# Optimization experiments

Measured on AMD Instinct MI355X. Metric: run time of the kernel, lower is better.

The kernel has to match this reference:

```python
import jax, jax.numpy as jnp
import numpy as np

EPS = 1e-5


def spectral_conv3d(x, w):
    # x: [B, C, X, Y, Z] real; w: [4, Cin, Cout, m1, m2, m3, 2] (4 frequency corners, real/imag)
    m1, m2, m3 = w.shape[3], w.shape[4], w.shape[5]
    wc = w[..., 0] + 1j * w[..., 1]
    X, Y, Z = x.shape[-3], x.shape[-2], x.shape[-1]
    xf = jnp.fft.rfftn(x, axes=(-3, -2, -1), norm="ortho")  # [B,C,X,Y,Z//2+1] complex
    mul = lambda a, b: jnp.einsum('bixyz,ioxyz->boxyz', a, b)
    out = jnp.zeros(xf.shape, dtype=xf.dtype)
    out = out.at[:, :, :m1, :m2, :m3].set(mul(xf[:, :, :m1, :m2, :m3], wc[0]))
    out = out.at[:, :, -m1:, :m2, :m3].set(mul(xf[:, :, -m1:, :m2, :m3], wc[1]))
    out = out.at[:, :, :m1, -m2:, :m3].set(mul(xf[:, :, :m1, -m2:, :m3], wc[2]))
    out = out.at[:, :, -m1:, -m2:, :m3].set(mul(xf[:, :, -m1:, -m2:, :m3], wc[3]))
    return jnp.fft.irfftn(out, s=(X, Y, Z), axes=(-3, -2, -1), norm="ortho")


def batchnorm3d(x, g, b):
    # training-mode BatchNorm3d: stats over (B, X, Y, Z) per channel, biased variance
    mean = jnp.mean(x, axis=(0, 2, 3, 4), keepdims=True)
    var = jnp.var(x, axis=(0, 2, 3, 4), keepdims=True)
    xhat = (x - mean) * jax.lax.rsqrt(var + EPS)
    return xhat * g[None, :, None, None, None] + b[None, :, None, None, None]


def setup_inputs() -> dict:
    key = jax.random.key(0)
    ks = jax.random.split(key, 12)
    B, X, Y, Z = 4, 64, 64, 64
    W, M = 32, 8
    scale = 1.0 / (W * W)
    return {
        "x": jax.random.normal(ks[0], (B, X, Y, Z, 3), dtype=jnp.float32),
        "fc0_w": jax.random.normal(ks[1], (W, 3), dtype=jnp.float32) * 0.3,
        "fc0_b": jax.random.normal(ks[2], (W,), dtype=jnp.float32) * 0.1,
        "sw": scale * jax.random.uniform(ks[3], (4, 4, W, W, M, M, M, 2), dtype=jnp.float32),
        "cw": jax.random.normal(ks[4], (4, W, W), dtype=jnp.float32) * (1.0 / np.sqrt(W)),
        "cb": jax.random.normal(ks[5], (4, W), dtype=jnp.float32) * 0.05,
        "gamma": jnp.ones((4, W), dtype=jnp.float32),
        "beta": jnp.zeros((4, W), dtype=jnp.float32),
        "fc1_w": jax.random.normal(ks[6], (128, W), dtype=jnp.float32) * (1.0 / np.sqrt(W)),
        "fc1_b": jax.random.normal(ks[7], (128,), dtype=jnp.float32) * 0.05,
        "fc2_w": jax.random.normal(ks[8], (1, 128), dtype=jnp.float32) * (1.0 / np.sqrt(128.0)),
        "fc2_b": jax.random.normal(ks[9], (1,), dtype=jnp.float32) * 0.05,
    }


def reference(x, fc0_w, fc0_b, sw, cw, cb, gamma, beta, fc1_w, fc1_b, fc2_w, fc2_b):
    # lift: [B,X,Y,Z,3] -> [B,X,Y,Z,W] -> [B,W,X,Y,Z]
    h = jnp.einsum('bxyzi,wi->bxyzw', x, fc0_w) + fc0_b
    h = jnp.transpose(h, (0, 4, 1, 2, 3))
    for i in range(4):
        x1 = spectral_conv3d(h, sw[i])
        x2 = jnp.einsum('bcxyz,oc->boxyz', h, cw[i]) + cb[i][None, :, None, None, None]
        h = batchnorm3d(x1 + x2, gamma[i], beta[i])
        if i < 3:
            h = jax.nn.relu(h)
    h = jnp.transpose(h, (0, 2, 3, 4, 1))  # [B,X,Y,Z,W]
    h = jax.nn.relu(jnp.einsum('bxyzw,fw->bxyzf', h, fc1_w) + fc1_b)
    out = jnp.einsum('bxyzf,of->bxyzo', h, fc2_w) + fc2_b
    return out
```

## Files before the change

kernel.cpp:

```cpp
#include <hip/hip_runtime.h>

#define TW_STEP 0.09817477042468103f

typedef __bf16 bf16x8 __attribute__((ext_vector_type(8)));
typedef __bf16 bf16x4 __attribute__((ext_vector_type(4)));
typedef __bf16 bf16x2 __attribute__((ext_vector_type(2)));
typedef float  f32x4  __attribute__((ext_vector_type(4)));

static constexpr size_t SZ_P   = (size_t)4*32*64*64*64*2;
static constexpr size_t SZ_A   = (size_t)4*32*8*64*64*8;
static constexpr size_t SZ_B2  = (size_t)4*32*8*16*64*8;
static constexpr size_t SZ_XF  = (size_t)4*32*8*16*16*8;
static constexpr size_t OFF_P  = 0;
static constexpr size_t OFF_A  = OFF_P + SZ_P;
static constexpr size_t OFF_B2 = OFF_A + SZ_A;
static constexpr size_t OFF_XF = OFF_B2 + SZ_B2;
static constexpr size_t OFF_YF = OFF_XF + SZ_XF;
static constexpr size_t OFF_TW  = OFF_YF + SZ_XF;
static constexpr size_t OFF_BNP = OFF_TW + 512;
static constexpr size_t OFF_W1B = OFF_BNP + 1024;
static constexpr size_t OFF_B1P = OFF_W1B + 8192;
static constexpr size_t OFF_WFZ = OFF_B1P + 512;
static constexpr size_t OFF_WZ  = OFF_WFZ + 4096;


__global__ void k_twinit(float2* tw, __bf16* wfz, __bf16* wz) {
    int t = threadIdx.x;
    if (t < 64) { float s, c; sincosf(TW_STEP * t, &s, &c); tw[t] = make_float2(c, s); }
    for (int e = t; e < 1024; e += 256) {
        int half = e >> 9, rem = e & 511, kg = rem >> 7, tt = (rem >> 3) & 15, j = e & 7;
        int z = half * 32 + kg * 8 + j, k = tt >> 1;
        float ang = TW_STEP * (float)((k * z) & 63);
        float val = (tt & 1) ? -sinf(ang) : cosf(ang);
        __bf16 hi = (__bf16)val;
        wfz[e] = hi;
        wfz[1024 + e] = (__bf16)(val - (float)hi);
    }
    for (int e = t; e < 2048; e += 256) {
        int z = e >> 5, tt = e & 31, k = tt >> 1;
        float ang = TW_STEP * (float)((k * z) & 63);
        float val;
        if (tt == 0) val = 1.f;
        else if (tt == 1) val = 0.f;
        else val = (tt & 1) ? (-2.f * sinf(ang)) : (2.f * cosf(ang));
        __bf16 hi = (__bf16)val;
        wz[e] = hi;
        wz[2048 + e] = (__bf16)(val - (float)hi);
    }
}

__global__ __launch_bounds__(256) void k_lift(const float* __restrict__ x,
                                              const float* __restrict__ w,
                                              const float* __restrict__ bias,
                                              __bf16* __restrict__ P) {
    int v = blockIdx.x * 256 + threadIdx.x;
    int z = v & 63, y = (v >> 6) & 63, xx = (v >> 12) & 63, b = v >> 18;
    float i0 = x[(size_t)v * 3 + 0], i1 = x[(size_t)v * 3 + 1], i2 = x[(size_t)v * 3 + 2];
#pragma unroll
    for (int c = 0; c < 32; c++) {
        float val = bias[c] + w[c * 3 + 0] * i0 + w[c * 3 + 1] * i1 + w[c * 3 + 2] * i2;
        P[(size_t)(((b * 32 + c) * 64 + xx) * 64 + y) * 64 + z] = (__bf16)val;
    }
}

__global__ __launch_bounds__(256) void k_zfwd(const __bf16* __restrict__ P,
                                              const __bf16* __restrict__ wfz,
                                              const float* __restrict__ bnp, int relu,
                                              __bf16* __restrict__ T1b) {
    int blk = blockIdx.x;
    int x = blk & 63, c = (blk >> 6) & 31, b = blk >> 11;
    __shared__ __bf16 hs2[64][72];
    __shared__ float ttmp[16][66];
    int tid = threadIdx.x, l = tid & 63, w = tid >> 6;
    {
        int y = tid >> 2, q = tid & 3;
        float scb = 1.f, shb = 0.f;
        if (bnp) { scb = bnp[c]; shb = bnp[32 + c]; }
        const __bf16* src = P + ((size_t)((b * 32 + c) * 64 + x) * 64 + y) * 64 + q * 16;
        bf16x8 v0 = ((const bf16x8*)src)[0], v1 = ((const bf16x8*)src)[1];
        bf16x8 o0, o1;
#pragma unroll
        for (int j = 0; j < 8; j++) {
            float a = (float)v0[j], bb = (float)v1[j];
            if (bnp) {
                a = fmaf(a, scb, shb); bb = fmaf(bb, scb, shb);
                if (relu) { a = fmaxf(a, 0.f); bb = fmaxf(bb, 0.f); }
            }
            o0[j] = (__bf16)a; o1[j] = (__bf16)bb;
        }
        *(bf16x8*)&hs2[y][q * 16] = o0;
        *(bf16x8*)&hs2[y][q * 16 + 8] = o1;
    }
    __syncthreads();
    int col = l & 15, kg = l >> 4;
    f32x4 acc = (f32x4){0.f, 0.f, 0.f, 0.f};
#pragma unroll
    for (int half = 0; half < 2; half++) {
        bf16x8 a = *(const bf16x8*)&hs2[w * 16 + col][half * 32 + kg * 8];
        const __bf16* wp = wfz + ((half * 4 + kg) * 16 + col) * 8;
        bf16x8 bh = *(const bf16x8*)wp;
        bf16x8 blo = *(const bf16x8*)(wp + 1024);
        acc = __builtin_amdgcn_mfma_f32_16x16x32_bf16(a, bh, acc, 0, 0, 0);
        acc = __builtin_amdgcn_mfma_f32_16x16x32_bf16(a, blo, acc, 0, 0, 0);
    }
#pragma unroll
    for (int r = 0; r < 4; r++) ttmp[col][w * 16 + kg * 4 + r] = acc[r];
    __syncthreads();
    if (tid < 128) {
        int k = tid >> 4, y0 = (tid & 15) * 4;
        float4 re4 = *(const float4*)&ttmp[2 * k][y0];
        float4 im4 = *(const float4*)&ttmp[2 * k + 1][y0];
        bf16x8 outv;
        outv[0] = (__bf16)re4.x; outv[1] = (__bf16)im4.x;
        outv[2] = (__bf16)re4.y; outv[3] = (__bf16)im4.y;
        outv[4] = (__bf16)re4.z; outv[5] = (__bf16)im4.z;
        outv[6] = (__bf16)re4.w; outv[7] = (__bf16)im4.w;
        size_t ob = (size_t)((b * 32 + c) * 8 + k) * 4096 + x * 64 + y0;
        *(bf16x8*)(T1b + ob * 2) = outv;
    }
}

__global__ __launch_bounds__(256) void k_dft2(const __bf16* __restrict__ in,
                                              __bf16* __restrict__ outb,
                                              float2* __restrict__ outf,
                                              const float2* __restrict__ gtw,
                                              int mode) {
    int rb = blockIdx.x * 16;
    __shared__ float2 rows[16][65];
    int tid = threadIdx.x;
#pragma unroll
    for (int k = 0; k < 4; k++) {
        int idx = tid + k * 256;
        int r = idx >> 6, y = idx & 63;
        bf16x2 p = ((const bf16x2*)in)[(size_t)(rb + r) * 64 + y];
        rows[r][y] = make_float2((float)p[0], (float)p[1]);
    }
    __syncthreads();
    int ki = tid & 15, r = tid >> 4;
    int f = ki < 8 ? ki : ki + 48;
    float2 w = gtw[f];
    float tc = 1.f, ts = 0.f;
    float ar = 0.f, ai = 0.f;
#pragma unroll 8
    for (int y = 0; y < 64; y++) {
        float2 v = rows[r][y];
        ar = fmaf(v.x, tc, ar); ar = fmaf(-v.y, ts, ar);
        ai = fmaf(v.x, ts, ai); ai = fmaf(v.y, tc, ai);
        float nc = fmaf(tc, w.x, ts * w.y);
        float ns = fmaf(ts, w.x, -tc * w.y);
        tc = nc; ts = ns;
    }
    int rg = rb + r;
    if (mode == 0) {
        union { __bf16 h[2]; unsigned u; } pk;
        pk.h[0] = (__bf16)ar; pk.h[1] = (__bf16)ai;
        ((unsigned*)outb)[(rg >> 6) * 1024 + ki * 64 + (rg & 63)] = pk.u;
    } else {
        outf[rg * 16 + ki] = make_float2(ar, ai);
    }
}

__global__ __launch_bounds__(128) void k_specmul(const float2* __restrict__ Xf,
                                                 const float* __restrict__ swl,
                                                 float2* __restrict__ Yf) {
    int m = blockIdx.x;
    int kxi = m & 15, kyi = (m >> 4) & 15, kz = m >> 8;
    int corner = (kxi >= 8 ? 1 : 0) + (kyi >= 8 ? 2 : 0);
    int mx = kxi & 7, my = kyi & 7;
    __shared__ float2 wsd[1024];
    __shared__ float2 xfs[128];
    int tid = threadIdx.x;
    const float* wb = swl + (size_t)corner * 1048576 + mx * 128 + my * 16 + kz * 2;
    for (int idx = tid; idx < 1024; idx += 128) {
        int i = idx >> 5, o = idx & 31;
        const float* p = wb + (size_t)i * 32768 + o * 1024;
        wsd[idx] = make_float2(p[0], p[1]);
    }
    {
        int b = tid >> 5, i = tid & 31;
        xfs[tid] = Xf[(((b * 32 + i) * 8 + kz) * 16 + kyi) * 16 + kxi];
    }
    __syncthreads();
    int b = tid >> 5, o = tid & 31;
    float ar = 0.f, ai = 0.f;
#pragma unroll
    for (int i = 0; i < 32; i++) {
        float2 xv = xfs[b * 32 + i];
        float2 wv = wsd[i * 32 + o];
        ar += xv.x * wv.x - xv.y * wv.y;
        ai += xv.x * wv.y + xv.y * wv.x;
    }
    const float s = 1.0f / 262144.0f;
    Yf[(((b * 32 + o) * 8 + kz) * 16 + kyi) * 16 + kxi] = make_float2(ar * s, ai * s);
}

__global__ __launch_bounds__(256) void k_xinv(const float2* __restrict__ Yf,
                                              float2* __restrict__ U1) {
    int blk = blockIdx.x;
    int kz = blk & 7, o = (blk >> 3) & 31, b = blk >> 8;
    __shared__ float2 yfs[16][17];
    __shared__ float2 tw[64];
    int tid = threadIdx.x;
    if (tid < 64) { float s, c; sincosf(TW_STEP * tid, &s, &c); tw[tid] = make_float2(c, s); }
    {
        int kyi = tid >> 4, kxi = tid & 15;
        yfs[kyi][kxi] = Yf[(size_t)((b * 32 + o) * 8 + kz) * 256 + tid];
    }
    __syncthreads();
    size_t base = (size_t)((b * 8 + kz) * 64) * 512 + o;
#pragma unroll
    for (int r = 0; r < 4; r++) {
        int idx = tid + r * 256;
        int x = idx >> 4, kyi = idx & 15;
        float ar = 0.f, ai = 0.f;
#pragma unroll
        for (int kxi = 0; kxi < 16; kxi++) {
            int f = kxi < 8 ? kxi : kxi + 48;
            float2 t = tw[(f * x) & 63];
            float2 v = yfs[kyi][kxi];
            ar += v.x * t.x - v.y * t.y;
            ai += v.x * t.y + v.y * t.x;
        }
        U1[base + (size_t)x * 512 + kyi * 32] = make_float2(ar, ai);
    }
}

__global__ __launch_bounds__(256) void k_fuse(__bf16* __restrict__ P,
                                              const float2* __restrict__ U1,
                                              const float* __restrict__ cwl,
                                              const float* __restrict__ cbl,
                                              const __bf16* __restrict__ wz,
                                              const float* __restrict__ bnp, int relu,
                                              float* __restrict__ part) {
    int blk = blockIdx.x;
    int yt = blk >> 8, bxi = blk & 255;
    int b = bxi >> 6, x = bxi & 63;
    int y0 = yt * 4;
    __shared__ __bf16 hs[256 * 40];
    __shared__ __bf16 u2b[4][32][20];
    __shared__ float2 twl[64];
    __shared__ float sredS[4][32], sredQ[4][32];
    int tid = threadIdx.x;
    int l = tid & 63, w = tid >> 6;
    if (tid < 64) { float s, c; sincosf(TW_STEP * tid, &s, &c); twl[tid] = make_float2(c, s); }
    __syncthreads();

    int col = l & 15, kg = l >> 4;
    bf16x8 cwf[2];
    float cbv[2];
#pragma unroll
    for (int nt = 0; nt < 2; nt++) {
        int o = nt * 16 + col;
        const float4* p4 = (const float4*)(cwl + o * 32 + kg * 8);
        float4 q0 = p4[0], q1 = p4[1];
        cwf[nt][0] = (__bf16)q0.x; cwf[nt][1] = (__bf16)q0.y;
        cwf[nt][2] = (__bf16)q0.z; cwf[nt][3] = (__bf16)q0.w;
        cwf[nt][4] = (__bf16)q1.x; cwf[nt][5] = (__bf16)q1.y;
        cwf[nt][6] = (__bf16)q1.z; cwf[nt][7] = (__bf16)q1.w;
        cbv[nt] = cbl[o];
    }

    {
        int c = tid >> 3, j = tid & 7;
        float scb = 1.f, shb = 0.f;
        if (bnp) { scb = bnp[c]; shb = bnp[32 + c]; }
        const __bf16* src = P + ((size_t)((b * 32 + c) * 64 + x) * 64 + y0) * 64 + j * 8;
#pragma unroll
        for (int q = 0; q < 4; q++) {
            bf16x8 v8 = *(const bf16x8*)(src + q * 64);
            float fv[8];
#pragma unroll
            for (int jj = 0; jj < 8; jj++) {
                float v = (float)v8[jj];
                if (bnp) { v = fmaf(v, scb, shb); if (relu) v = fmaxf(v, 0.f); }
                fv[jj] = v;
            }
#pragma unroll
            for (int s = 0; s < 8; s++) {
                int jr = (s + j) & 7;
                hs[(q * 64 + j * 8 + jr) * 40 + c] = (__bf16)fv[jr];
            }
        }
    }
    {
        int o = tid & 31, kz = tid >> 5;
        const float2* u1p = U1 + (size_t)((b * 8 + kz) * 64 + x) * 512 + o;
        float ar[4] = {0.f, 0.f, 0.f, 0.f}, ai[4] = {0.f, 0.f, 0.f, 0.f};
#pragma unroll
        for (int kyi = 0; kyi < 16; kyi++) {
            float2 u = u1p[kyi * 32];
            int f = kyi < 8 ? kyi : kyi + 48;
#pragma unroll
            for (int yy = 0; yy < 4; yy++) {
                float2 t = twl[(f * (y0 + yy)) & 63];
                ar[yy] = fmaf(u.x, t.x, ar[yy]); ar[yy] = fmaf(-u.y, t.y, ar[yy]);
                ai[yy] = fmaf(u.x, t.y, ai[yy]); ai[yy] = fmaf(u.y, t.x, ai[yy]);
            }
        }
#pragma unroll
        for (int yy = 0; yy < 4; yy++) {
            union { __bf16 h[2]; unsigned u; } pk;
            pk.h[0] = (__bf16)ar[yy]; pk.h[1] = (__bf16)ai[yy];
            *(unsigned*)&u2b[yy][o][2 * kz] = pk.u;
        }
    }
    __syncthreads();

    f32x4 acc[4][2];
#pragma unroll
    for (int i = 0; i < 4; i++) {
        bf16x8 a = *(const bf16x8*)&hs[((w * 4 + i) * 16 + col) * 40 + kg * 8];
#pragma unroll
        for (int nt = 0; nt < 2; nt++) {
            acc[i][nt] = (f32x4){0.f, 0.f, 0.f, 0.f};
            acc[i][nt] = __builtin_amdgcn_mfma_f32_16x16x32_bf16(a, cwf[nt], acc[i][nt], 0, 0, 0);
        }
    }
    {
        bf16x8 u2f[2];
#pragma unroll
        for (int nt = 0; nt < 2; nt++) {
            bf16x8 v = (bf16x8){(__bf16)0.f, (__bf16)0.f, (__bf16)0.f, (__bf16)0.f,
                                (__bf16)0.f, (__bf16)0.f, (__bf16)0.f, (__bf16)0.f};
            if (kg < 2) {
                bf16x4 lo = *(const bf16x4*)&u2b[w][nt * 16 + col][kg * 8];
                bf16x4 hi = *(const bf16x4*)&u2b[w][nt * 16 + col][kg * 8 + 4];
                v[0] = lo[0]; v[1] = lo[1]; v[2] = lo[2]; v[3] = lo[3];
                v[4] = hi[0]; v[5] = hi[1]; v[6] = hi[2]; v[7] = hi[3];
            }
            u2f[nt] = v;
        }
#pragma unroll
        for (int i = 0; i < 4; i++) {
            int z = i * 16 + col;
            const __bf16* wp = wz + z * 32 + kg * 8;
            bf16x8 wzh = *(const bf16x8*)wp;
            bf16x8 wzl = *(const bf16x8*)(wp + 2048);
#pragma unroll
            for (int nt = 0; nt < 2; nt++) {
                acc[i][nt] = __builtin_amdgcn_mfma_f32_16x16x32_bf16(wzh, u2f[nt], acc[i][nt], 0, 0, 0);
                acc[i][nt] = __builtin_amdgcn_mfma_f32_16x16x32_bf16(wzl, u2f[nt], acc[i][nt], 0, 0, 0);
            }
        }
    }

    float sacc[2] = {0.f, 0.f}, ssacc[2] = {0.f, 0.f};
#pragma unroll
    for (int nt = 0; nt < 2; nt++) {
        int o = nt * 16 + col;
        __bf16* dstb = P + ((size_t)((b * 32 + o) * 64 + x) * 64 + (y0 + w)) * 64;
#pragma unroll
        for (int i = 0; i < 4; i++) {
            int z0s = i * 16 + kg * 4;
            bf16x4 outv;
#pragma unroll
            for (int r = 0; r < 4; r++) {
                float f = acc[i][nt][r] + cbv[nt];
                sacc[nt] += f;
                ssacc[nt] = fmaf(f, f, ssacc[nt]);
                outv[r] = (__bf16)f;
            }
            *(bf16x4*)(dstb + z0s) = outv;
        }
    }
#pragma unroll
    for (int nt = 0; nt < 2; nt++) {
        sacc[nt] += __shfl_xor(sacc[nt], 16, 64);
        sacc[nt] += __shfl_xor(sacc[nt], 32, 64);
        ssacc[nt] += __shfl_xor(ssacc[nt], 16, 64);
        ssacc[nt] += __shfl_xor(ssacc[nt], 32, 64);
    }
    if (l < 16) {
        sredS[w][col] = sacc[0]; sredS[w][16 + col] = sacc[1];
        sredQ[w][col] = ssacc[0]; sredQ[w][16 + col] = ssacc[1];
    }
    __syncthreads();
    if (tid < 32) {
        float S = sredS[0][tid] + sredS[1][tid] + sredS[2][tid] + sredS[3][tid];
        float SS = sredQ[0][tid] + sredQ[1][tid] + sredQ[2][tid] + sredQ[3][tid];
        part[((size_t)tid * 4096 + blk) * 2 + 0] = S;
        part[((size_t)tid * 4096 + blk) * 2 + 1] = SS;
    }
}

__global__ __launch_bounds__(256) void k_red2(const float* __restrict__ part,
                                              const float* __restrict__ gamma,
                                              const float* __restrict__ beta,
                                              float* __restrict__ bnp) {
    int c = blockIdx.x;
    int tid = threadIdx.x;
    const float2* pc = (const float2*)(part + (size_t)c * 8192);
    float s = 0.f, ss = 0.f;
#pragma unroll
    for (int q = 0; q < 16; q++) { float2 v = pc[tid * 16 + q]; s += v.x; ss += v.y; }
#pragma unroll
    for (int d = 32; d; d >>= 1) { s += __shfl_down(s, d, 64); ss += __shfl_down(ss, d, 64); }
    __shared__ float ws[8];
    if ((tid & 63) == 0) { ws[(tid >> 6) * 2] = s; ws[(tid >> 6) * 2 + 1] = ss; }
    __syncthreads();
    if (tid == 0) {
        double S = (double)ws[0] + ws[2] + ws[4] + ws[6];
        double SS = (double)ws[1] + ws[3] + ws[5] + ws[7];
        const double invN = 1.0 / 1048576.0;
        double mean = S * invN;
        double var = SS * invN - mean * mean;
        float scl = gamma[c] * rsqrtf((float)var + 1e-5f);
        bnp[c] = scl;
        bnp[32 + c] = beta[c] - (float)mean * scl;
    }
}

__global__ void k_prep(const float* __restrict__ w1, const float* __restrict__ b1,
                       const float* __restrict__ bnp,
                       __bf16* __restrict__ w1b, float* __restrict__ b1p) {
    int f = threadIdx.x;
    if (f >= 128) return;
    float acc = b1[f];
#pragma unroll
    for (int c = 0; c < 32; c++) {
        float wv = w1[f * 32 + c];
        w1b[f * 32 + c] = (__bf16)(wv * bnp[c]);
        acc = fmaf(wv, bnp[32 + c], acc);
    }
    b1p[f] = acc;
}

__global__ __launch_bounds__(256) void k_head(const __bf16* __restrict__ P,
                                              const __bf16* __restrict__ w1b,
                                              const float* __restrict__ b1p,
                                              const float* __restrict__ w2,
                                              const float* __restrict__ b2,
                                              float* __restrict__ out) {
    __shared__ __bf16 hs[64 * 40];
    int tid = threadIdx.x;
    int b = blockIdx.x >> 9;
    int r0 = (blockIdx.x & 511) * 512;
    int l = tid & 63;
    int w = tid >> 6;
    int col = l & 15, kg = l >> 4, hi = l >> 4;

    bf16x8 afr[8];
    f32x4 b1q[8], w2q[8];
    {
#pragma unroll
        for (int nt = 0; nt < 8; nt++) {
            afr[nt] = *(const bf16x8*)(w1b + (nt * 16 + col) * 32 + kg * 8);
            b1q[nt] = ((const f32x4*)b1p)[nt * 4 + hi];
            w2q[nt] = ((const f32x4*)w2)[nt * 4 + hi];
        }
    }
    float b2v = b2[0];
    int sc_c = tid & 31, sc_j = tid >> 5;
    const __bf16* srcb = P + (size_t)(b * 32 + sc_c) * 262144 + r0 + sc_j * 8;

    for (int t = 0; t < 8; t++) {
        {
            bf16x8 v8 = *(const bf16x8*)(srcb + t * 64);
#pragma unroll
            for (int s = 0; s < 8; s++) {
                int jr = (s + sc_j * 4) & 7;
                hs[(sc_j * 8 + jr) * 40 + sc_c] = v8[jr];
            }
        }
        __syncthreads();
        bf16x8 hfr = *(const bf16x8*)&hs[(w * 16 + col) * 40 + kg * 8];
        f32x4 acc[8];
#pragma unroll
        for (int nt = 0; nt < 8; nt++) {
            acc[nt] = (f32x4){0.f, 0.f, 0.f, 0.f};
            acc[nt] = __builtin_amdgcn_mfma_f32_16x16x32_bf16(afr[nt], hfr, acc[nt], 0, 0, 0);
        }
        float s = 0.f;
#pragma unroll
        for (int nt = 0; nt < 8; nt++) {
#pragma unroll
            for (int r = 0; r < 4; r++) {
                float val = fmaxf(acc[nt][r] + b1q[nt][r], 0.f);
                s = fmaf(w2q[nt][r], val, s);
            }
        }
        s += __shfl_xor(s, 16, 64);
        s += __shfl_xor(s, 32, 64);
        if (l < 16)
            out[b * 262144 + r0 + t * 64 + w * 16 + l] = s + b2v;
        __syncthreads();
    }
}

extern "C" void kernel_launch(void* const* d_in, const int* in_sizes, int n_in,
                              void* d_out, int out_size, void* d_ws, size_t ws_size,
                              hipStream_t stream) {
    const float* x     = (const float*)d_in[0];
    const float* fc0_w = (const float*)d_in[1];
    const float* fc0_b = (const float*)d_in[2];
    const float* sw    = (const float*)d_in[3];
    const float* cw    = (const float*)d_in[4];
    const float* cb    = (const float*)d_in[5];
    const float* gamma = (const float*)d_in[6];
    const float* beta  = (const float*)d_in[7];
    const float* fc1_w = (const float*)d_in[8];
    const float* fc1_b = (const float*)d_in[9];
    const float* fc2_w = (const float*)d_in[10];
    const float* fc2_b = (const float*)d_in[11];

    char* ws = (char*)d_ws;
    __bf16* P    = (__bf16*)(ws + OFF_P);
    __bf16* T1b  = (__bf16*)(ws + OFF_A);
    __bf16* T2b  = (__bf16*)(ws + OFF_B2);
    float2* Bb   = (float2*)(ws + OFF_B2);
    float2* Xf   = (float2*)(ws + OFF_XF);
    float2* Yf   = (float2*)(ws + OFF_YF);
    float*  part = (float*)(ws + OFF_XF);
    float2* gtw  = (float2*)(ws + OFF_TW);
    float*  bnp  = (float*)(ws + OFF_BNP);
    __bf16* w1b  = (__bf16*)(ws + OFF_W1B);
    float*  b1p  = (float*)(ws + OFF_B1P);
    __bf16* wfz  = (__bf16*)(ws + OFF_WFZ);
    __bf16* wz   = (__bf16*)(ws + OFF_WZ);

    k_twinit<<<1, 256, 0, stream>>>(gtw, wfz, wz);
    k_lift<<<4096, 256, 0, stream>>>(x, fc0_w, fc0_b, P);

    for (int i = 0; i < 4; i++) {
        const float* bprev = (i == 0) ? nullptr : (bnp + (i - 1) * 64);
        int relu = (i > 0) ? 1 : 0;
        k_zfwd<<<8192, 256, 0, stream>>>(P, wfz, bprev, relu, T1b);
        k_dft2<<<4096, 256, 0, stream>>>(T1b, T2b, nullptr, gtw, 0);
        k_dft2<<<1024, 256, 0, stream>>>(T2b, nullptr, Xf, gtw, 1);
        k_specmul<<<2048, 128, 0, stream>>>(Xf, sw + (size_t)i * 4194304, Yf);
        k_xinv<<<1024, 256, 0, stream>>>(Yf, Bb);
        k_fuse<<<4096, 256, 0, stream>>>(P, Bb, cw + i * 1024, cb + i * 32, wz, bprev, relu, part);
        k_red2<<<32, 256, 0, stream>>>(part, gamma + i * 32, beta + i * 32, bnp + i * 64);
    }

    k_prep<<<1, 128, 0, stream>>>(fc1_w, fc1_b, bnp + 3 * 64, w1b, b1p);
    k_head<<<2048, 256, 0, stream>>>(P, w1b, b1p, fc2_w, fc2_b, (float*)d_out);
}
```

Baseline: 506.2 us.

## Compute inverse-Y DFT in k_fuse with bf16 MFMA and split twiddles

The inverse DFT along Y inside k_fuse, previously a scalar FMA loop over 16 modes and 4 outputs per thread using an LDS twiddle table, is now a matrix multiply. U1 spectra are staged in LDS as bf16, and a twiddle matrix is built with sincosf and split into high and low bf16 parts. Two 16x16x32 bf16 MFMAs per tile produce the results. This moves scalar ALU work onto matrix cores, but adds LDS staging, a second sync region and rounding of U1 to bf16, which lowers the precision of the input spectra.

```diff
diff --git a/kernel.cpp b/kernel.cpp
--- a/kernel.cpp
+++ b/kernel.cpp
@@ -237,15 +237,14 @@
     int b = bxi >> 6, x = bxi & 63;
     int y0 = yt * 4;
     __shared__ __bf16 hs[256 * 40];
+    __shared__ __bf16 u1b[256 * 36];
+    __shared__ __bf16 aY[2 * 16 * 40];
     __shared__ __bf16 u2b[4][32][20];
-    __shared__ float2 twl[64];
     __shared__ float sredS[4][32], sredQ[4][32];
     int tid = threadIdx.x;
     int l = tid & 63, w = tid >> 6;
-    if (tid < 64) { float s, c; sincosf(TW_STEP * tid, &s, &c); twl[tid] = make_float2(c, s); }
-    __syncthreads();
-
     int col = l & 15, kg = l >> 4;
+
     bf16x8 cwf[2];
     float cbv[2];
 #pragma unroll
@@ -285,23 +284,54 @@
     {
         int o = tid & 31, kz = tid >> 5;
         const float2* u1p = U1 + (size_t)((b * 8 + kz) * 64 + x) * 512 + o;
-        float ar[4] = {0.f, 0.f, 0.f, 0.f}, ai[4] = {0.f, 0.f, 0.f, 0.f};
+        __bf16 tmp[32];
 #pragma unroll
         for (int kyi = 0; kyi < 16; kyi++) {
             float2 u = u1p[kyi * 32];
-            int f = kyi < 8 ? kyi : kyi + 48;
-#pragma unroll
-            for (int yy = 0; yy < 4; yy++) {
-                float2 t = twl[(f * (y0 + yy)) & 63];
-                ar[yy] = fmaf(u.x, t.x, ar[yy]); ar[yy] = fmaf(-u.y, t.y, ar[yy]);
-                ai[yy] = fmaf(u.x, t.y, ai[yy]); ai[yy] = fmaf(u.y, t.x, ai[yy]);
-            }
-        }
-#pragma unroll
-        for (int yy = 0; yy < 4; yy++) {
-            union { __bf16 h[2]; unsigned u; } pk;
-            pk.h[0] = (__bf16)ar[yy]; pk.h[1] = (__bf16)ai[yy];
-            *(unsigned*)&u2b[yy][o][2 * kz] = pk.u;
+            tmp[2 * kyi] = (__bf16)u.x; tmp[2 * kyi + 1] = (__bf16)u.y;
+        }
+        __bf16* rowp = &u1b[(kz * 32 + o) * 36];
+#pragma unroll
+        for (int q = 0; q < 8; q++)
+            *(bf16x4*)(rowp + q * 4) = *(bf16x4*)&tmp[q * 4];
+    }
+    {
+        int m = tid >> 5, kap = tid & 31;
+        int yy = m >> 1, p = m & 1, kyi = kap >> 1, q = kap & 1;
+        int f = kyi < 8 ? kyi : kyi + 48;
+        int y = y0 + yy;
+        float sv, cv;
+        sincosf(TW_STEP * (float)((f * y) & 63), &sv, &cv);
+        float val = (p == 0) ? (q == 0 ? cv : -sv) : (q == 0 ? sv : cv);
+        __bf16 hi = (__bf16)val;
+        aY[m * 40 + kap] = hi;
+        aY[640 + m * 40 + kap] = (__bf16)(val - (float)hi);
+    }
+    __syncthreads();
+
+    {
+        bf16x8 ah = *(const bf16x8*)&aY[col * 40 + kg * 8];
+        bf16x8 al = *(const bf16x8*)&aY[640 + col * 40 + kg * 8];
+#pragma unroll
+        for (int ti = 0; ti < 4; ti++) {
+            int tile = w * 4 + ti;
+            int kz = tile >> 1, oh = tile & 1;
+            const __bf16* rowp = &u1b[(kz * 32 + oh * 16 + col) * 36 + kg * 8];
+            bf16x4 b0 = *(const bf16x4*)rowp;
+            bf16x4 b1 = *(const bf16x4*)(rowp + 4);
+            bf16x8 bfv;
+            bfv[0] = b0[0]; bfv[1] = b0[1]; bfv[2] = b0[2]; bfv[3] = b0[3];
+            bfv[4] = b1[0]; bfv[5] = b1[1]; bfv[6] = b1[2]; bfv[7] = b1[3];
+            f32x4 d = (f32x4){0.f, 0.f, 0.f, 0.f};
+            d = __builtin_amdgcn_mfma_f32_16x16x32_bf16(ah, bfv, d, 0, 0, 0);
+            d = __builtin_amdgcn_mfma_f32_16x16x32_bf16(al, bfv, d, 0, 0, 0);
+            if (kg < 2) {
+#pragma unroll
+                for (int r = 0; r < 4; r++) {
+                    int yy = kg * 2 + (r >> 1);
+                    u2b[yy][oh * 16 + col][2 * kz + (r & 1)] = (__bf16)d[r];
+                }
+            }
         }
     }
     __syncthreads();
```

Result: no change. 512.9 us (+1.3%).
